# Performance work log

Hardware: AMD Instinct MI355X
Metric: run time of the kernel (lower is better)

Reference implementation:

```python
import jax, jax.numpy as jnp
import numpy as np
import math

B, L, D, H, FACTOR = 4, 2048, 256, 8, 5
DH = D // H

def setup_inputs() -> dict:
    key = jax.random.key(0)
    ks = jax.random.split(key, 12)
    s = 1.0 / math.sqrt(D)
    return {
        "q": jax.random.normal(ks[0], (B, L, D), jnp.float32),
        "k": jax.random.normal(ks[1], (B, L, D), jnp.float32),
        "v": jax.random.normal(ks[2], (B, L, D), jnp.float32),
        "Wq": jax.random.normal(ks[3], (D, D), jnp.float32) * s,
        "bq": jax.random.normal(ks[4], (D,), jnp.float32) * s,
        "Wk": jax.random.normal(ks[5], (D, D), jnp.float32) * s,
        "bk": jax.random.normal(ks[6], (D,), jnp.float32) * s,
        "Wv": jax.random.normal(ks[7], (D, D), jnp.float32) * s,
        "bv": jax.random.normal(ks[8], (D,), jnp.float32) * s,
        "Wc": jax.random.normal(ks[9], (D, D), jnp.float32) * s,
        "bc": jax.random.normal(ks[10], (D,), jnp.float32) * s,
        "index_sample": jax.random.randint(ks[11], (L,), 0, L),  # U_part = min(5*L*ceil(log1p(L)), L) = L
    }

def reference(q, k, v, Wq, bq, Wk, bk, Wv, bv, Wc, bc, index_sample):
    # projections (torch Linear: x @ W^T + b)
    qp = q @ Wq.T + bq
    kp = k @ Wk.T + bk
    vp = v @ Wv.T + bv
    # NOTE: original reshapes q with a raw view (no transpose), k/v via split()
    q4 = qp.reshape(B, H, L, DH)                       # faithful to q.view(B, H, L, dh)
    k4 = kp.reshape(B, L, H, DH).transpose(0, 2, 1, 3)
    v4 = vp.reshape(B, L, H, DH).transpose(0, 2, 1, 3)
    qf = q4.reshape(B * H, L, DH)
    kf = k4.reshape(B * H, L, DH)
    vf = v4.reshape(B * H, L, DH)
    # random K sampling (with replacement); U_part == L here
    K_sample = kf[:, index_sample, :]                  # [BH, L, dh]
    QK = jnp.einsum('bld,bud->blu', qf, K_sample)      # [BH, L, L]
    M = QK.max(axis=-1) - QK.sum(axis=-1) / L          # sparsity measure [BH, L]
    u = min(FACTOR * math.ceil(math.log1p(L)), L)      # = 40
    _, top_idx = jax.lax.top_k(-M, u)                  # topk(..., largest=False)
    Q_red = jnp.take_along_axis(qf, top_idx[:, :, None], axis=1)  # [BH, u, dh]
    scores = jnp.einsum('bud,bld->bul', Q_red, kf) / math.sqrt(DH)
    probs = jax.nn.softmax(scores, axis=-1)
    out = jnp.einsum('bul,bld->bud', probs, vf)        # [BH, u, dh]
    out = out.reshape(B, H, u, DH).transpose(0, 2, 1, 3).reshape(B, u, D)
    return out @ Wc.T + bc
```

## Files before the change

kernel.cpp:

```cpp
#include <hip/hip_runtime.h>
#include <math.h>

#define B_ 4
#define L_ 2048
#define D_ 256
#define H_ 8
#define DH_ 32
#define NH_ 32
#define U_ 40
#define LD_ 524288
#define NCH_ 16

typedef __attribute__((ext_vector_type(8))) short short8;
typedef __attribute__((ext_vector_type(4))) float floatx4;

static __device__ __forceinline__ unsigned long long ullmin_(unsigned long long a, unsigned long long b) {
    return a < b ? a : b;
}
static __device__ __forceinline__ unsigned short f2bf_rne(float x) {
    unsigned u = __float_as_uint(x);
    unsigned r = u + 0x7FFFu + ((u >> 16) & 1u);
    return (unsigned short)(r >> 16);
}
static __device__ __forceinline__ float bf2f(unsigned short h) {
    return __uint_as_float(((unsigned)h) << 16);
}

__global__ __launch_bounds__(256) void wsplit(const float* __restrict__ Wq,
                                              const float* __restrict__ Wk,
                                              const float* __restrict__ Wv,
                                              unsigned short* __restrict__ Whs,
                                              unsigned short* __restrict__ Wms,
                                              unsigned short* __restrict__ Wls) {
    const int g = blockIdx.x * 256 + threadIdx.x;
    const int mat = g >> 14;
    const int rem = g & 16383;
    const int col = rem >> 6;
    const int k4 = rem & 63;
    const float* W = (mat == 0) ? Wq : (mat == 1) ? Wk : Wv;
    const float4 x = *(const float4*)(W + (size_t)col * 256 + k4 * 4);
    float xs[4] = {x.x, x.y, x.z, x.w};
    unsigned short hv[4], mv[4], lv[4];
#pragma unroll
    for (int j = 0; j < 4; ++j) {
        hv[j] = f2bf_rne(xs[j]);
        const float e1 = xs[j] - bf2f(hv[j]);
        mv[j] = f2bf_rne(e1);
        const float e2 = e1 - bf2f(mv[j]);
        lv[j] = f2bf_rne(e2);
    }
    const int colblk = col >> 6, c64 = col & 63;
    const int nt = c64 >> 4, cin = c64 & 15;
    const int kt = k4 >> 3, kin = (k4 & 7) * 4;
    const size_t o = ((((size_t)mat * 4 + colblk) * 8 + kt) << 11) + nt * 512 + cin * 32 + kin;
    *(ushort4*)(Whs + o) = make_ushort4(hv[0], hv[1], hv[2], hv[3]);
    *(ushort4*)(Wms + o) = make_ushort4(mv[0], mv[1], mv[2], mv[3]);
    *(ushort4*)(Wls + o) = make_ushort4(lv[0], lv[1], lv[2], lv[3]);
}

__global__ __launch_bounds__(256) void gemm_proj(const float* __restrict__ q,
                                                 const float* __restrict__ k,
                                                 const float* __restrict__ v,
                                                 const unsigned short* __restrict__ Whs,
                                                 const unsigned short* __restrict__ Wms,
                                                 const unsigned short* __restrict__ Wls,
                                                 const float* __restrict__ bq,
                                                 const float* __restrict__ bk,
                                                 const float* __restrict__ bv,
                                                 float* __restrict__ qp,
                                                 float* __restrict__ kp,
                                                 float* __restrict__ vp) {
    const int mat = blockIdx.z;
    const float* X = (mat == 0) ? q : (mat == 1) ? k : v;
    const float* bias = (mat == 0) ? bq : (mat == 1) ? bk : bv;
    float* Y = (mat == 0) ? qp : (mat == 1) ? kp : vp;

    const int t = threadIdx.x;
    const int w = t >> 6, lane = t & 63;
    const int lq = lane & 15, quad = lane >> 4;
    const int colBase = blockIdx.y * 64;
    const int rowBaseW = blockIdx.x * 128 + w * 32;

    const size_t pbase = ((size_t)mat * 4 + blockIdx.y) << 14;
    const unsigned short* Whb = Whs + pbase;
    const unsigned short* Wmb = Wms + pbase;
    const unsigned short* Wlb = Wls + pbase;
    const int fo = lq * 32 + quad * 8;

    floatx4 acc[2][4];
#pragma unroll
    for (int mt = 0; mt < 2; ++mt)
#pragma unroll
        for (int nt = 0; nt < 4; ++nt) acc[mt][nt] = (floatx4){0.f, 0.f, 0.f, 0.f};

#pragma unroll 2
    for (int kt = 0; kt < 8; ++kt) {
        short8 Bh[4], Bm[4], Bl[4];
#pragma unroll
        for (int j = 0; j < 4; ++j) {
            Bh[j] = *(const short8*)(Whb + (kt << 11) + j * 512 + fo);
            Bm[j] = *(const short8*)(Wmb + (kt << 11) + j * 512 + fo);
            Bl[j] = *(const short8*)(Wlb + (kt << 11) + j * 512 + fo);
        }
#pragma unroll
        for (int mt = 0; mt < 2; ++mt) {
            const int m = rowBaseW + mt * 16 + lq;
            short8 Ah, Am, Al;
            {
                const float* xr = X + (size_t)m * 256 + kt * 32 + quad * 8;
                const float4 x0 = *(const float4*)xr;
                const float4 x1 = *(const float4*)(xr + 4);
                float xs[8] = {x0.x, x0.y, x0.z, x0.w, x1.x, x1.y, x1.z, x1.w};
#pragma unroll
                for (int j = 0; j < 8; ++j) {
                    const unsigned short h = f2bf_rne(xs[j]);
                    const float e1 = xs[j] - bf2f(h);
                    const unsigned short md = f2bf_rne(e1);
                    const float e2 = e1 - bf2f(md);
                    Ah[j] = (short)h;
                    Am[j] = (short)md;
                    Al[j] = (short)f2bf_rne(e2);
                }
            }
#pragma unroll
            for (int j = 0; j < 4; ++j) {
                floatx4 a = acc[mt][j];
                a = __builtin_amdgcn_mfma_f32_16x16x32_bf16(Am, Bm[j], a, 0, 0, 0);
                a = __builtin_amdgcn_mfma_f32_16x16x32_bf16(Ah, Bl[j], a, 0, 0, 0);
                a = __builtin_amdgcn_mfma_f32_16x16x32_bf16(Al, Bh[j], a, 0, 0, 0);
                a = __builtin_amdgcn_mfma_f32_16x16x32_bf16(Ah, Bm[j], a, 0, 0, 0);
                a = __builtin_amdgcn_mfma_f32_16x16x32_bf16(Am, Bh[j], a, 0, 0, 0);
                a = __builtin_amdgcn_mfma_f32_16x16x32_bf16(Ah, Bh[j], a, 0, 0, 0);
                acc[mt][j] = a;
            }
        }
    }

#pragma unroll
    for (int mt = 0; mt < 2; ++mt)
#pragma unroll
        for (int nt = 0; nt < 4; ++nt) {
            const int c = colBase + nt * 16 + lq;
            const float bv_ = bias[c];
#pragma unroll
            for (int r = 0; r < 4; ++r) {
                const int mr = rowBaseW + mt * 16 + quad * 4 + r;
                Y[(size_t)mr * 256 + c] = acc[mt][nt][r] + bv_;
            }
        }
}

__global__ __launch_bounds__(256) void gemm_out(const float* __restrict__ X,
                                                const float* __restrict__ Wc,
                                                const float* __restrict__ bias,
                                                float* __restrict__ Y) {
    const int t = threadIdx.x;
    const int rowBase = blockIdx.x * 16;
    const int colBase = blockIdx.y * 64;
    const int col = colBase + (t & 63);
    const int rq = (t >> 6) * 4;

    __shared__ float Xs[16][256];
#pragma unroll
    for (int e = t; e < 1024; e += 256) {
        const int r = e >> 6, kq = (e & 63) * 4;
        *(float4*)&Xs[r][kq] = *(const float4*)(X + (size_t)(rowBase + r) * 256 + kq);
    }
    __syncthreads();

    const float* wr = Wc + (size_t)col * 256;
    float acc[4] = {0.f, 0.f, 0.f, 0.f};
#pragma unroll 8
    for (int k = 0; k < 256; k += 4) {
        const float4 wv = *(const float4*)(wr + k);
#pragma unroll
        for (int r = 0; r < 4; ++r) {
            acc[r] = fmaf(Xs[rq + r][k + 0], wv.x, acc[r]);
            acc[r] = fmaf(Xs[rq + r][k + 1], wv.y, acc[r]);
            acc[r] = fmaf(Xs[rq + r][k + 2], wv.z, acc[r]);
            acc[r] = fmaf(Xs[rq + r][k + 3], wv.w, acc[r]);
        }
    }

    const float bv = bias[col];
#pragma unroll
    for (int r = 0; r < 4; ++r)
        Y[(size_t)(rowBase + rq + r) * 256 + col] = acc[r] + bv;
}

__global__ __launch_bounds__(256) void kconv_ksum(const float* __restrict__ kp,
                                                  const int* __restrict__ idx,
                                                  unsigned short* __restrict__ Khi,
                                                  unsigned short* __restrict__ Klo,
                                                  float* __restrict__ Ksum32) {
    const int blk = blockIdx.x;
    const int i = blk >> 5, uc = blk & 31;
    const int b = i >> 3, h = i & 7;
    const int t = threadIdx.x;
    const int dq = (t & 7) * 4;
    const int ur = t >> 3;

    __shared__ float part[32][36];
    float ksum[4] = {0.f, 0.f, 0.f, 0.f};

#pragma unroll
    for (int p = 0; p < 2; ++p) {
        int u = uc * 64 + p * 32 + ur;
        const float4 x = *(const float4*)(kp + (size_t)b * LD_ + (size_t)idx[u] * D_ + h * DH_ + dq);
        float xs[4] = {x.x, x.y, x.z, x.w};
        unsigned short hv[4], lv[4];
#pragma unroll
        for (int j = 0; j < 4; ++j) {
            ksum[j] += xs[j];
            hv[j] = f2bf_rne(xs[j]);
            lv[j] = f2bf_rne(xs[j] - bf2f(hv[j]));
        }
        size_t o = ((size_t)i * 2048 + u) * 32 + dq;
        *(ushort4*)(Khi + o) = make_ushort4(hv[0], hv[1], hv[2], hv[3]);
        *(ushort4*)(Klo + o) = make_ushort4(lv[0], lv[1], lv[2], lv[3]);
    }
#pragma unroll
    for (int j = 0; j < 4; ++j) part[ur][dq + j] = ksum[j];
    __syncthreads();
    if (t < 32) {
        float s = 0.f;
#pragma unroll 8
        for (int u2 = 0; u2 < 32; ++u2) s += part[u2][t];
        Ksum32[(size_t)blk * 32 + t] = s;
    }
}

__global__ __launch_bounds__(256) void mpart_mfma(const float* __restrict__ qp,
                                                  const unsigned short* __restrict__ Khi,
                                                  const unsigned short* __restrict__ Klo,
                                                  const float* __restrict__ Ksum32,
                                                  float* __restrict__ Mv,
                                                  float* __restrict__ Qmean) {
    const int blk = blockIdx.x;
    const int i = blk >> 5;
    const int lg = blk & 31;
    const int t = threadIdx.x;
    const int w = t >> 6;
    const int lane = t & 63;
    const int lq = lane & 15;
    const int quad = lane >> 4;

    __shared__ float ssum[32];
    __shared__ float red[4][64];
    if (t < 32) {
        float s = 0.f;
#pragma unroll 8
        for (int uc = 0; uc < 32; ++uc) s += Ksum32[((size_t)i * 32 + uc) * 32 + t];
        ssum[t] = s;
    }

    short8 Ah[4], Al[4];
#pragma unroll
    for (int lt = 0; lt < 4; ++lt) {
        const int l = lg * 64 + lt * 16 + lq;
        const float* qrow = qp + ((size_t)i * 2048 + l) * 32 + quad * 8;
        float4 x0 = *(const float4*)(qrow);
        float4 x1 = *(const float4*)(qrow + 4);
        float xs[8] = {x0.x, x0.y, x0.z, x0.w, x1.x, x1.y, x1.z, x1.w};
#pragma unroll
        for (int j = 0; j < 8; ++j) {
            unsigned short h = f2bf_rne(xs[j]);
            unsigned short lo = f2bf_rne(xs[j] - bf2f(h));
            Ah[lt][j] = (short)h;
            Al[lt][j] = (short)lo;
        }
    }

    floatx4 rmax[4];
#pragma unroll
    for (int lt = 0; lt < 4; ++lt)
        rmax[lt] = (floatx4){-INFINITY, -INFINITY, -INFINITY, -INFINITY};

    const size_t kfrag = ((size_t)i * 2048 + w * 512 + lq) * 32 + quad * 8;
    const unsigned short* ph = Khi + kfrag;
    const unsigned short* pl = Klo + kfrag;
#pragma unroll 2
    for (int s = 0; s < 32; ++s) {
        short8 Bh = *(const short8*)(ph + (size_t)s * 512);
        short8 Bl = *(const short8*)(pl + (size_t)s * 512);
#pragma unroll
        for (int lt = 0; lt < 4; ++lt) {
            floatx4 acc = (floatx4){0.f, 0.f, 0.f, 0.f};
            acc = __builtin_amdgcn_mfma_f32_16x16x32_bf16(Al[lt], Bh, acc, 0, 0, 0);
            acc = __builtin_amdgcn_mfma_f32_16x16x32_bf16(Ah[lt], Bl, acc, 0, 0, 0);
            acc = __builtin_amdgcn_mfma_f32_16x16x32_bf16(Ah[lt], Bh, acc, 0, 0, 0);
#pragma unroll
            for (int r = 0; r < 4; ++r) rmax[lt][r] = fmaxf(rmax[lt][r], acc[r]);
        }
    }

#pragma unroll
    for (int lt = 0; lt < 4; ++lt)
#pragma unroll
        for (int r = 0; r < 4; ++r) {
            float v = rmax[lt][r];
#pragma unroll
            for (int off = 1; off < 16; off <<= 1)
                v = fmaxf(v, __shfl_xor(v, off, 64));
            rmax[lt][r] = v;
        }
    if (lq == 0) {
#pragma unroll
        for (int lt = 0; lt < 4; ++lt)
#pragma unroll
            for (int r = 0; r < 4; ++r)
                red[w][lt * 16 + quad * 4 + r] = rmax[lt][r];
    }
    __syncthreads();
    if (t < 64) {
        const int l = lg * 64 + t;
        float m = fmaxf(fmaxf(red[0][t], red[1][t]), fmaxf(red[2][t], red[3][t]));
        const float4* q4 = (const float4*)(qp + ((size_t)i * 2048 + l) * 32);
        const float4* s4 = (const float4*)ssum;
        float qs = 0.f;
#pragma unroll
        for (int z = 0; z < 8; ++z) {
            float4 a = q4[z];
            float4 c = s4[z];
            qs = fmaf(a.x, c.x, qs);
            qs = fmaf(a.y, c.y, qs);
            qs = fmaf(a.z, c.z, qs);
            qs = fmaf(a.w, c.w, qs);
        }
        const float qm = qs * (1.0f / 2048.0f);
        Qmean[(size_t)i * 2048 + l] = qm;
        Mv[(size_t)i * 2048 + l] = m - qm;
    }
}

__global__ __launch_bounds__(256) void topk64_kernel(const float* __restrict__ Mv,
                                                     int* __restrict__ candIdx) {
    const int i = blockIdx.x;
    const int t = threadIdx.x;
    unsigned long long keys[8];
    __shared__ unsigned long long wred[4];
#pragma unroll
    for (int j = 0; j < 8; ++j) {
        const int l = t + 256 * j;
        unsigned u32 = __float_as_uint(Mv[(size_t)i * 2048 + l]);
        u32 = (u32 & 0x80000000u) ? ~u32 : (u32 | 0x80000000u);
        keys[j] = ((unsigned long long)u32 << 32) | (unsigned)l;
    }
    for (int it = 0; it < 64; ++it) {
        unsigned long long best = keys[0];
#pragma unroll
        for (int j = 1; j < 8; ++j) best = ullmin_(best, keys[j]);
#pragma unroll
        for (int off = 1; off < 64; off <<= 1)
            best = ullmin_(best, __shfl_xor(best, off, 64));
        if ((t & 63) == 0) wred[t >> 6] = best;
        __syncthreads();
        const unsigned long long m = ullmin_(ullmin_(wred[0], wred[1]), ullmin_(wred[2], wred[3]));
        if (t == 0) candIdx[i * 64 + it] = (int)(m & 0xffffffffu);
#pragma unroll
        for (int j = 0; j < 8; ++j)
            if (keys[j] == m) keys[j] = ~0ULL;
        __syncthreads();
    }
}

__global__ __launch_bounds__(256) void refine_kernel(const float* __restrict__ qp,
                                                     const float* __restrict__ kp,
                                                     const int* __restrict__ idx,
                                                     const int* __restrict__ candIdx,
                                                     float* __restrict__ refPart) {
    const int blk = blockIdx.x;
    const int i = blk >> 3, c = blk & 7;
    const int b = i >> 3, h = i & 7;
    const int t = threadIdx.x;
    __shared__ float qc[64][40];
    __shared__ float Ks[128][40];

    {
        const int cand = t >> 2, dp = (t & 3) * 8;
        const int l = candIdx[i * 64 + cand];
        const float* src = qp + ((size_t)i * 2048 + l) * 32 + dp;
        *(float4*)&qc[cand][dp] = *(const float4*)(src);
        *(float4*)&qc[cand][dp + 4] = *(const float4*)(src + 4);
    }
    __syncthreads();

    const int cand = t >> 2, usub = t & 3;
    float qv[32];
#pragma unroll
    for (int z = 0; z < 8; ++z) {
        float4 a = *(const float4*)&qc[cand][z * 4];
        qv[4 * z] = a.x; qv[4 * z + 1] = a.y; qv[4 * z + 2] = a.z; qv[4 * z + 3] = a.w;
    }

    float m = -INFINITY;
    for (int s = 0; s < 2; ++s) {
        {
            const int r = t >> 1, half = t & 1;
            const int u = c * 256 + s * 128 + r;
            const float* krow = kp + (size_t)b * LD_ + (size_t)idx[u] * D_ + h * DH_ + half * 16;
#pragma unroll
            for (int z = 0; z < 4; ++z)
                *(float4*)&Ks[r][half * 16 + z * 4] = *(const float4*)(krow + z * 4);
        }
        __syncthreads();
        for (int ur = usub; ur < 128; ur += 4) {
            float a0 = 0, a1 = 0, a2 = 0, a3 = 0;
#pragma unroll
            for (int z = 0; z < 8; ++z) {
                float4 kv = *(const float4*)&Ks[ur][z * 4];
                a0 = fmaf(qv[4 * z], kv.x, a0);
                a1 = fmaf(qv[4 * z + 1], kv.y, a1);
                a2 = fmaf(qv[4 * z + 2], kv.z, a2);
                a3 = fmaf(qv[4 * z + 3], kv.w, a3);
            }
            m = fmaxf(m, (a0 + a1) + (a2 + a3));
        }
        __syncthreads();
    }
    m = fmaxf(m, __shfl_xor(m, 1, 64));
    m = fmaxf(m, __shfl_xor(m, 2, 64));
    if ((t & 3) == 0) refPart[((size_t)i * 8 + c) * 64 + cand] = m;
}

__global__ __launch_bounds__(64) void select40_kernel(const int* __restrict__ candIdx,
                                                      const float* __restrict__ refPart,
                                                      const float* __restrict__ Qmean,
                                                      int* __restrict__ topIdx) {
    const int i = blockIdx.x;
    const int t = threadIdx.x;
    const int l = candIdx[i * 64 + t];
    float m = -INFINITY;
#pragma unroll
    for (int c = 0; c < 8; ++c) m = fmaxf(m, refPart[((size_t)i * 8 + c) * 64 + t]);
    float Mex = m - Qmean[(size_t)i * 2048 + l];
    unsigned u32 = __float_as_uint(Mex);
    u32 = (u32 & 0x80000000u) ? ~u32 : (u32 | 0x80000000u);
    unsigned long long key = ((unsigned long long)u32 << 32) | (unsigned)l;
    for (int it = 0; it < 40; ++it) {
        unsigned long long k2 = key;
#pragma unroll
        for (int off = 1; off < 64; off <<= 1) k2 = ullmin_(k2, __shfl_xor(k2, off, 64));
        if (key == k2) {
            topIdx[i * 40 + it] = l;
            key = ~0ULL;
        }
    }
}

#define SCP2 136
#define VSP 36

__global__ __launch_bounds__(320) void attn_part(const float* __restrict__ qp,
                                                 const float* __restrict__ kp,
                                                 const float* __restrict__ vp,
                                                 const int* __restrict__ topIdx,
                                                 float* __restrict__ mPart,
                                                 float* __restrict__ sPart,
                                                 float* __restrict__ oPart) {
    const int blk = blockIdx.x;
    const int i = blk >> 4, c = blk & 15;
    const int b = i >> 3, h = i & 7;
    const int t = threadIdx.x;

    __shared__ float Qs[40][32];
    __shared__ float Vs[128][VSP];
    __shared__ float sc[40][SCP2];
    __shared__ float mred[40], sred[40];

    {
        const int r = t >> 3, qq = t & 7;
        const int lq = topIdx[i * 40 + r];
        *(float4*)&Qs[r][qq * 4] = *(const float4*)(qp + ((size_t)i * 2048 + lq) * 32 + qq * 4);
    }
    for (int e = t; e < 1024; e += 320) {
        const int r = e >> 3, qq = e & 7;
        *(float4*)&Vs[r][qq * 4] =
            *(const float4*)(vp + (size_t)b * LD_ + (size_t)(c * 128 + r) * 256 + h * 32 + qq * 4);
    }
    __syncthreads();

    const float scale = 0.17677669529663687f;

    if (t < 256) {
        const int r = t >> 1;
        const int j0 = (t & 1) * 20;
        const float* kr = kp + (size_t)b * LD_ + (size_t)(c * 128 + r) * 256 + h * 32;
        float kv[32];
#pragma unroll
        for (int z = 0; z < 8; ++z) {
            float4 x = *(const float4*)(kr + z * 4);
            kv[4 * z] = x.x; kv[4 * z + 1] = x.y; kv[4 * z + 2] = x.z; kv[4 * z + 3] = x.w;
        }
#pragma unroll 4
        for (int jj = 0; jj < 20; ++jj) {
            const int j = j0 + jj;
            float a0 = 0, a1 = 0, a2 = 0, a3 = 0;
#pragma unroll
            for (int z = 0; z < 8; ++z) {
                const float4 q4 = *(const float4*)&Qs[j][z * 4];
                a0 = fmaf(kv[4 * z], q4.x, a0);
                a1 = fmaf(kv[4 * z + 1], q4.y, a1);
                a2 = fmaf(kv[4 * z + 2], q4.z, a2);
                a3 = fmaf(kv[4 * z + 3], q4.w, a3);
            }
            sc[j][r] = ((a0 + a1) + (a2 + a3)) * scale;
        }
    }
    __syncthreads();

    {
        const int w = t >> 6, lane = t & 63;
#pragma unroll
        for (int rr = 0; rr < 8; ++rr) {
            const int j = w * 8 + rr;
            float x0 = sc[j][lane], x1 = sc[j][lane + 64];
            float m = fmaxf(x0, x1);
#pragma unroll
            for (int off = 1; off < 64; off <<= 1) m = fmaxf(m, __shfl_xor(m, off, 64));
            const float e0 = __expf(x0 - m), e1 = __expf(x1 - m);
            sc[j][lane] = e0; sc[j][lane + 64] = e1;
            float s = e0 + e1;
#pragma unroll
            for (int off = 1; off < 64; off <<= 1) s += __shfl_xor(s, off, 64);
            if (lane == 0) { mred[j] = m; sred[j] = s; }
        }
    }
    __syncthreads();

    {
        const int j = t >> 3, qq = t & 7;
        float4 acc = make_float4(0.f, 0.f, 0.f, 0.f);
        for (int l = 0; l < 128; ++l) {
            const float p = sc[j][l];
            const float4 v4 = *(const float4*)&Vs[l][qq * 4];
            acc.x = fmaf(p, v4.x, acc.x);
            acc.y = fmaf(p, v4.y, acc.y);
            acc.z = fmaf(p, v4.z, acc.z);
            acc.w = fmaf(p, v4.w, acc.w);
        }
        const size_t o = (size_t)(i * NCH_ + c) * 40 + j;
        *(float4*)&oPart[o * 32 + qq * 4] = acc;
        if (qq == 0) { mPart[o] = mred[j]; sPart[o] = sred[j]; }
    }
}

__global__ __launch_bounds__(256) void attn_combine(const float* __restrict__ mPart,
                                                    const float* __restrict__ sPart,
                                                    const float* __restrict__ oPart,
                                                    float* __restrict__ attnOut) {
    const int i = blockIdx.x;
    const int b = i >> 3, h = i & 7;
    const int t = threadIdx.x;
    for (int e = t; e < 1280; e += 256) {
        const int j = e >> 5, d = e & 31;
        float mv[NCH_];
        float M = -INFINITY;
#pragma unroll
        for (int c = 0; c < NCH_; ++c) {
            mv[c] = mPart[(size_t)(i * NCH_ + c) * 40 + j];
            M = fmaxf(M, mv[c]);
        }
        float S = 0.f, O = 0.f;
#pragma unroll
        for (int c = 0; c < NCH_; ++c) {
            const float sc_ = __expf(mv[c] - M);
            const size_t o = (size_t)(i * NCH_ + c) * 40 + j;
            S = fmaf(sPart[o], sc_, S);
            O = fmaf(oPart[o * 32 + d], sc_, O);
        }
        attnOut[((size_t)b * 40 + j) * 256 + h * 32 + d] = O / S;
    }
}

extern "C" void kernel_launch(void* const* d_in, const int* in_sizes, int n_in,
                              void* d_out, int out_size, void* d_ws, size_t ws_size,
                              hipStream_t stream) {
    const float* q  = (const float*)d_in[0];
    const float* k  = (const float*)d_in[1];
    const float* v  = (const float*)d_in[2];
    const float* Wq = (const float*)d_in[3];
    const float* bq = (const float*)d_in[4];
    const float* Wk = (const float*)d_in[5];
    const float* bk = (const float*)d_in[6];
    const float* Wv = (const float*)d_in[7];
    const float* bv = (const float*)d_in[8];
    const float* Wc = (const float*)d_in[9];
    const float* bc = (const float*)d_in[10];
    const int* idx  = (const int*)d_in[11];
    float* out = (float*)d_out;

    char* w = (char*)d_ws;
    float*          qp      = (float*)(w);
    float*          kp      = (float*)(w + (8u << 20));
    float*          vp      = (float*)(w + (16u << 20));
    unsigned short* Khi     = (unsigned short*)(w + (24u << 20));
    unsigned short* Klo     = (unsigned short*)(w + (28u << 20));
    float*          Mv      = (float*)(w + (32u << 20));
    float*          Qmean   = (float*)(w + (32u << 20) + (256u << 10));
    float*          Ksum32  = (float*)(w + (32u << 20) + (512u << 10));
    int*            candIdx = (int*)  (w + (32u << 20) + (640u << 10));
    int*            topIdx  = (int*)  (w + (32u << 20) + (648u << 10));
    float*          refPart = (float*)(w + (32u << 20) + (656u << 10));
    float*          attnOut = (float*)(w + (32u << 20) + (720u << 10));
    unsigned short* Whs     = (unsigned short*)(w + (40u << 20));
    unsigned short* Wms     = (unsigned short*)(w + (40u << 20) + (512u << 10));
    unsigned short* Wls     = (unsigned short*)(w + (41u << 20));
    float*          mPart   = (float*)(w + (24u << 20));
    float*          sPart   = (float*)(w + (24u << 20) + (128u << 10));
    float*          oPart   = (float*)(w + (24u << 20) + (256u << 10));

    hipLaunchKernelGGL(wsplit, dim3(192), dim3(256), 0, stream, Wq, Wk, Wv, Whs, Wms, Wls);
    hipLaunchKernelGGL(gemm_proj, dim3(64, 4, 3), dim3(256), 0, stream,
                       q, k, v, Whs, Wms, Wls, bq, bk, bv, qp, kp, vp);
    hipLaunchKernelGGL(kconv_ksum, dim3(1024), dim3(256), 0, stream, kp, idx, Khi, Klo, Ksum32);
    hipLaunchKernelGGL(mpart_mfma, dim3(1024), dim3(256), 0, stream, qp, Khi, Klo, Ksum32, Mv, Qmean);
    hipLaunchKernelGGL(topk64_kernel, dim3(32), dim3(256), 0, stream, Mv, candIdx);
    hipLaunchKernelGGL(refine_kernel, dim3(256), dim3(256), 0, stream, qp, kp, idx, candIdx, refPart);
    hipLaunchKernelGGL(select40_kernel, dim3(32), dim3(64), 0, stream, candIdx, refPart, Qmean, topIdx);
    hipLaunchKernelGGL(attn_part, dim3(512), dim3(320), 0, stream, qp, kp, vp, topIdx, mPart, sPart, oPart);
    hipLaunchKernelGGL(attn_combine, dim3(32), dim3(256), 0, stream, mPart, sPart, oPart, attnOut);
    hipLaunchKernelGGL(gemm_out, dim3(10, 4), dim3(256), 0, stream, attnOut, Wc, bc, out);
}
```

Baseline: 252.0 us.

## Radix-select top-64, fold select40 into attn_part, widen attn_combine grid

Replaces the 64-iteration serial argmin top-k with a 4-level 8-bit radix histogram select, followed by a short tie-resolution loop over keys equal to the threshold. The select40 step now runs inside attn_part, with one wave doing the selection while the other waves load V, which removes one kernel launch and the topIdx round-trip. attn_combine is spread over 160 blocks instead of 32 to raise parallelism. The risk is that all 16 chunk blocks per head redundantly repeat the select40 work, and radix tie handling has to reproduce the old ordering exactly.

```diff
diff --git a/kernel.cpp b/kernel.cpp
--- a/kernel.cpp
+++ b/kernel.cpp
@@ -150,44 +150,6 @@
         }
 }
 
-__global__ __launch_bounds__(256) void gemm_out(const float* __restrict__ X,
-                                                const float* __restrict__ Wc,
-                                                const float* __restrict__ bias,
-                                                float* __restrict__ Y) {
-    const int t = threadIdx.x;
-    const int rowBase = blockIdx.x * 16;
-    const int colBase = blockIdx.y * 64;
-    const int col = colBase + (t & 63);
-    const int rq = (t >> 6) * 4;
-
-    __shared__ float Xs[16][256];
-#pragma unroll
-    for (int e = t; e < 1024; e += 256) {
-        const int r = e >> 6, kq = (e & 63) * 4;
-        *(float4*)&Xs[r][kq] = *(const float4*)(X + (size_t)(rowBase + r) * 256 + kq);
-    }
-    __syncthreads();
-
-    const float* wr = Wc + (size_t)col * 256;
-    float acc[4] = {0.f, 0.f, 0.f, 0.f};
-#pragma unroll 8
-    for (int k = 0; k < 256; k += 4) {
-        const float4 wv = *(const float4*)(wr + k);
-#pragma unroll
-        for (int r = 0; r < 4; ++r) {
-            acc[r] = fmaf(Xs[rq + r][k + 0], wv.x, acc[r]);
-            acc[r] = fmaf(Xs[rq + r][k + 1], wv.y, acc[r]);
-            acc[r] = fmaf(Xs[rq + r][k + 2], wv.z, acc[r]);
-            acc[r] = fmaf(Xs[rq + r][k + 3], wv.w, acc[r]);
-        }
-    }
-
-    const float bv = bias[col];
-#pragma unroll
-    for (int r = 0; r < 4; ++r)
-        Y[(size_t)(rowBase + rq + r) * 256 + col] = acc[r] + bv;
-}
-
 __global__ __launch_bounds__(256) void kconv_ksum(const float* __restrict__ kp,
                                                   const int* __restrict__ idx,
                                                   unsigned short* __restrict__ Khi,
@@ -333,35 +295,104 @@
     }
 }
 
-__global__ __launch_bounds__(256) void topk64_kernel(const float* __restrict__ Mv,
-                                                     int* __restrict__ candIdx) {
+__global__ __launch_bounds__(256) void topk64_fast(const float* __restrict__ Mv,
+                                                   int* __restrict__ candIdx) {
     const int i = blockIdx.x;
     const int t = threadIdx.x;
+    const int w = t >> 6, lane = t & 63;
+
+    __shared__ unsigned hist[256];
+    __shared__ unsigned sh_prefix, sh_selBelow;
+    __shared__ unsigned cnt;
+    __shared__ int candLds[64];
+    __shared__ unsigned long long wred[4];
+
+    unsigned v[8];
+#pragma unroll
+    for (int j = 0; j < 8; ++j) {
+        const unsigned u = __float_as_uint(Mv[(size_t)i * 2048 + t + 256 * j]);
+        v[j] = (u & 0x80000000u) ? ~u : (u | 0x80000000u);
+    }
+
+    if (t == 0) { sh_prefix = 0u; sh_selBelow = 0u; cnt = 0u; }
+
+    for (int level = 0; level < 4; ++level) {
+        const int shift = 24 - 8 * level;
+        __syncthreads();
+        const unsigned prefHi = sh_prefix;
+        const unsigned selB = sh_selBelow;
+        const unsigned mask = (level == 0) ? 0u : (0xFFFFFFFFu << (shift + 8));
+        hist[t] = 0u;
+        __syncthreads();
+#pragma unroll
+        for (int j = 0; j < 8; ++j)
+            if ((v[j] & mask) == prefHi)
+                atomicAdd(&hist[(v[j] >> shift) & 255u], 1u);
+        __syncthreads();
+        if (t < 64) {
+            const unsigned c0 = hist[t * 4 + 0], c1 = hist[t * 4 + 1];
+            const unsigned c2 = hist[t * 4 + 2], c3 = hist[t * 4 + 3];
+            const unsigned i0 = c0, i1 = c0 + c1, i2 = i1 + c2, i3 = i2 + c3;
+            unsigned x = i3;
+#pragma unroll
+            for (int off = 1; off < 64; off <<= 1) {
+                const unsigned y = __shfl_up(x, off, 64);
+                if (t >= off) x += y;
+            }
+            const unsigned excl = x - i3;
+            const unsigned r = 64u - selB;
+            const unsigned long long ball = __ballot(x >= r);
+            const int flane = __ffsll(ball) - 1;
+            if (t == flane) {
+                unsigned k, ce;
+                if (excl + i0 >= r)      { k = 0u; ce = excl; }
+                else if (excl + i1 >= r) { k = 1u; ce = excl + i0; }
+                else if (excl + i2 >= r) { k = 2u; ce = excl + i1; }
+                else                     { k = 3u; ce = excl + i2; }
+                sh_prefix = prefHi | (((unsigned)t * 4u + k) << shift);
+                sh_selBelow = selB + ce;
+            }
+        }
+    }
+    __syncthreads();
+    const unsigned thr = sh_prefix;
+    const unsigned selB = sh_selBelow;
+    const int rem = 64 - (int)selB;
+
     unsigned long long keys[8];
-    __shared__ unsigned long long wred[4];
 #pragma unroll
     for (int j = 0; j < 8; ++j) {
         const int l = t + 256 * j;
-        unsigned u32 = __float_as_uint(Mv[(size_t)i * 2048 + l]);
-        u32 = (u32 & 0x80000000u) ? ~u32 : (u32 | 0x80000000u);
-        keys[j] = ((unsigned long long)u32 << 32) | (unsigned)l;
-    }
-    for (int it = 0; it < 64; ++it) {
+        if (v[j] < thr) {
+            const unsigned p = atomicAdd(&cnt, 1u);
+            candLds[p] = l;
+            keys[j] = ~0ULL;
+        } else if (v[j] == thr) {
+            keys[j] = ((unsigned long long)v[j] << 32) | (unsigned)l;
+        } else {
+            keys[j] = ~0ULL;
+        }
+    }
+    __syncthreads();
+
+    for (int it = 0; it < rem; ++it) {
         unsigned long long best = keys[0];
 #pragma unroll
         for (int j = 1; j < 8; ++j) best = ullmin_(best, keys[j]);
 #pragma unroll
         for (int off = 1; off < 64; off <<= 1)
             best = ullmin_(best, __shfl_xor(best, off, 64));
-        if ((t & 63) == 0) wred[t >> 6] = best;
+        if (lane == 0) wred[w] = best;
         __syncthreads();
         const unsigned long long m = ullmin_(ullmin_(wred[0], wred[1]), ullmin_(wred[2], wred[3]));
-        if (t == 0) candIdx[i * 64 + it] = (int)(m & 0xffffffffu);
+        if (t == 0) candLds[selB + it] = (int)(m & 0xffffffffu);
 #pragma unroll
         for (int j = 0; j < 8; ++j)
             if (keys[j] == m) keys[j] = ~0ULL;
         __syncthreads();
     }
+
+    if (t < 64) candIdx[i * 64 + t] = candLds[t];
 }
 
 __global__ __launch_bounds__(256) void refine_kernel(const float* __restrict__ qp,
@@ -423,38 +454,15 @@
     if ((t & 3) == 0) refPart[((size_t)i * 8 + c) * 64 + cand] = m;
 }
 
-__global__ __launch_bounds__(64) void select40_kernel(const int* __restrict__ candIdx,
-                                                      const float* __restrict__ refPart,
-                                                      const float* __restrict__ Qmean,
-                                                      int* __restrict__ topIdx) {
-    const int i = blockIdx.x;
-    const int t = threadIdx.x;
-    const int l = candIdx[i * 64 + t];
-    float m = -INFINITY;
-#pragma unroll
-    for (int c = 0; c < 8; ++c) m = fmaxf(m, refPart[((size_t)i * 8 + c) * 64 + t]);
-    float Mex = m - Qmean[(size_t)i * 2048 + l];
-    unsigned u32 = __float_as_uint(Mex);
-    u32 = (u32 & 0x80000000u) ? ~u32 : (u32 | 0x80000000u);
-    unsigned long long key = ((unsigned long long)u32 << 32) | (unsigned)l;
-    for (int it = 0; it < 40; ++it) {
-        unsigned long long k2 = key;
-#pragma unroll
-        for (int off = 1; off < 64; off <<= 1) k2 = ullmin_(k2, __shfl_xor(k2, off, 64));
-        if (key == k2) {
-            topIdx[i * 40 + it] = l;
-            key = ~0ULL;
-        }
-    }
-}
-
 #define SCP2 136
 #define VSP 36
 
 __global__ __launch_bounds__(320) void attn_part(const float* __restrict__ qp,
                                                  const float* __restrict__ kp,
                                                  const float* __restrict__ vp,
-                                                 const int* __restrict__ topIdx,
+                                                 const int* __restrict__ candIdx,
+                                                 const float* __restrict__ refPart,
+                                                 const float* __restrict__ Qmean,
                                                  float* __restrict__ mPart,
                                                  float* __restrict__ sPart,
                                                  float* __restrict__ oPart) {
@@ -467,16 +475,39 @@
     __shared__ float Vs[128][VSP];
     __shared__ float sc[40][SCP2];
     __shared__ float mred[40], sred[40];
+    __shared__ int topl[40];
+
+    if (t < 64) {
+        const int l = candIdx[i * 64 + t];
+        float m = -INFINITY;
+#pragma unroll
+        for (int cc = 0; cc < 8; ++cc) m = fmaxf(m, refPart[((size_t)i * 8 + cc) * 64 + t]);
+        float Mex = m - Qmean[(size_t)i * 2048 + l];
+        unsigned u32 = __float_as_uint(Mex);
+        u32 = (u32 & 0x80000000u) ? ~u32 : (u32 | 0x80000000u);
+        unsigned long long key = ((unsigned long long)u32 << 32) | (unsigned)l;
+        for (int it = 0; it < 40; ++it) {
+            unsigned long long k2 = key;
+#pragma unroll
+            for (int off = 1; off < 64; off <<= 1) k2 = ullmin_(k2, __shfl_xor(k2, off, 64));
+            if (key == k2) {
+                topl[it] = l;
+                key = ~0ULL;
+            }
+        }
+    } else {
+        for (int e = t - 64; e < 1024; e += 256) {
+            const int r = e >> 3, qq = e & 7;
+            *(float4*)&Vs[r][qq * 4] =
+                *(const float4*)(vp + (size_t)b * LD_ + (size_t)(c * 128 + r) * 256 + h * 32 + qq * 4);
+        }
+    }
+    __syncthreads();
 
     {
         const int r = t >> 3, qq = t & 7;
-        const int lq = topIdx[i * 40 + r];
+        const int lq = topl[r];
         *(float4*)&Qs[r][qq * 4] = *(const float4*)(qp + ((size_t)i * 2048 + lq) * 32 + qq * 4);
-    }
-    for (int e = t; e < 1024; e += 320) {
-        const int r = e >> 3, qq = e & 7;
-        *(float4*)&Vs[r][qq * 4] =
-            *(const float4*)(vp + (size_t)b * LD_ + (size_t)(c * 128 + r) * 256 + h * 32 + qq * 4);
     }
     __syncthreads();
 
@@ -549,28 +580,66 @@
                                                     const float* __restrict__ sPart,
                                                     const float* __restrict__ oPart,
                                                     float* __restrict__ attnOut) {
-    const int i = blockIdx.x;
-    const int b = i >> 3, h = i & 7;
-    const int t = threadIdx.x;
-    for (int e = t; e < 1280; e += 256) {
-        const int j = e >> 5, d = e & 31;
-        float mv[NCH_];
-        float M = -INFINITY;
-#pragma unroll
-        for (int c = 0; c < NCH_; ++c) {
-            mv[c] = mPart[(size_t)(i * NCH_ + c) * 40 + j];
-            M = fmaxf(M, mv[c]);
-        }
-        float S = 0.f, O = 0.f;
-#pragma unroll
-        for (int c = 0; c < NCH_; ++c) {
-            const float sc_ = __expf(mv[c] - M);
-            const size_t o = (size_t)(i * NCH_ + c) * 40 + j;
-            S = fmaf(sPart[o], sc_, S);
-            O = fmaf(oPart[o * 32 + d], sc_, O);
-        }
-        attnOut[((size_t)b * 40 + j) * 256 + h * 32 + d] = O / S;
-    }
+    const int blk = blockIdx.x;
+    const int b = blk / 40, j = blk - b * 40;
+    const int t = threadIdx.x;
+    const int h = t >> 5, d = t & 31;
+    const int i = b * 8 + h;
+
+    float mv[NCH_];
+    float M = -INFINITY;
+#pragma unroll
+    for (int c = 0; c < NCH_; ++c) {
+        mv[c] = mPart[(size_t)(i * NCH_ + c) * 40 + j];
+        M = fmaxf(M, mv[c]);
+    }
+    float S = 0.f, O = 0.f;
+#pragma unroll
+    for (int c = 0; c < NCH_; ++c) {
+        const float sc_ = __expf(mv[c] - M);
+        const size_t o = (size_t)(i * NCH_ + c) * 40 + j;
+        S = fmaf(sPart[o], sc_, S);
+        O = fmaf(oPart[o * 32 + d], sc_, O);
+    }
+    attnOut[((size_t)b * 40 + j) * 256 + h * 32 + d] = O / S;
+}
+
+__global__ __launch_bounds__(256) void gemm_out(const float* __restrict__ X,
+                                                const float* __restrict__ Wc,
+                                                const float* __restrict__ bias,
+                                                float* __restrict__ Y) {
+    const int t = threadIdx.x;
+    const int rowBase = blockIdx.x * 16;
+    const int colBase = blockIdx.y * 64;
+    const int col = colBase + (t & 63);
+    const int rq = (t >> 6) * 4;
+
+    __shared__ float Xs[16][256];
+#pragma unroll
+    for (int e = t; e < 1024; e += 256) {
+        const int r = e >> 6, kq = (e & 63) * 4;
+        *(float4*)&Xs[r][kq] = *(const float4*)(X + (size_t)(rowBase + r) * 256 + kq);
+    }
+    __syncthreads();
+
+    const float* wr = Wc + (size_t)col * 256;
+    float acc[4] = {0.f, 0.f, 0.f, 0.f};
+#pragma unroll 8
+    for (int k = 0; k < 256; k += 4) {
+        const float4 wv = *(const float4*)(wr + k);
+#pragma unroll
+        for (int r = 0; r < 4; ++r) {
+            acc[r] = fmaf(Xs[rq + r][k + 0], wv.x, acc[r]);
+            acc[r] = fmaf(Xs[rq + r][k + 1], wv.y, acc[r]);
+            acc[r] = fmaf(Xs[rq + r][k + 2], wv.z, acc[r]);
+            acc[r] = fmaf(Xs[rq + r][k + 3], wv.w, acc[r]);
+        }
+    }
+
+    const float bv = bias[col];
+#pragma unroll
+    for (int r = 0; r < 4; ++r)
+        Y[(size_t)(rowBase + rq + r) * 256 + col] = acc[r] + bv;
 }
 
 extern "C" void kernel_launch(void* const* d_in, const int* in_sizes, int n_in,
@@ -600,7 +669,6 @@
     float*          Qmean   = (float*)(w + (32u << 20) + (256u << 10));
     float*          Ksum32  = (float*)(w + (32u << 20) + (512u << 10));
     int*            candIdx = (int*)  (w + (32u << 20) + (640u << 10));
-    int*            topIdx  = (int*)  (w + (32u << 20) + (648u << 10));
     float*          refPart = (float*)(w + (32u << 20) + (656u << 10));
     float*          attnOut = (float*)(w + (32u << 20) + (720u << 10));
     unsigned short* Whs     = (unsigned short*)(w + (40u << 20));
@@ -615,10 +683,10 @@
                        q, k, v, Whs, Wms, Wls, bq, bk, bv, qp, kp, vp);
     hipLaunchKernelGGL(kconv_ksum, dim3(1024), dim3(256), 0, stream, kp, idx, Khi, Klo, Ksum32);
     hipLaunchKernelGGL(mpart_mfma, dim3(1024), dim3(256), 0, stream, qp, Khi, Klo, Ksum32, Mv, Qmean);
-    hipLaunchKernelGGL(topk64_kernel, dim3(32), dim3(256), 0, stream, Mv, candIdx);
+    hipLaunchKernelGGL(topk64_fast, dim3(32), dim3(256), 0, stream, Mv, candIdx);
     hipLaunchKernelGGL(refine_kernel, dim3(256), dim3(256), 0, stream, qp, kp, idx, candIdx, refPart);
-    hipLaunchKernelGGL(select40_kernel, dim3(32), dim3(64), 0, stream, candIdx, refPart, Qmean, topIdx);
-    hipLaunchKernelGGL(attn_part, dim3(512), dim3(320), 0, stream, qp, kp, vp, topIdx, mPart, sPart, oPart);
-    hipLaunchKernelGGL(attn_combine, dim3(32), dim3(256), 0, stream, mPart, sPart, oPart, attnOut);
+    hipLaunchKernelGGL(attn_part, dim3(512), dim3(320), 0, stream,
+                       qp, kp, vp, candIdx, refPart, Qmean, mPart, sPart, oPart);
+    hipLaunchKernelGGL(attn_combine, dim3(160), dim3(256), 0, stream, mPart, sPart, oPart, attnOut);
     hipLaunchKernelGGL(gemm_out, dim3(10, 4), dim3(256), 0, stream, attnOut, Wc, bc, out);
 }
```

Measured after the change: 215.3 us. -14.6%, faster.
